# Kernel tuning notes

Hardware: AMD Instinct MI355X
Metric: run time of the kernel (lower is better)

## Reference

```python
import jax, jax.numpy as jnp
import numpy as np
import math

N, C, T, V = 32, 64, 400, 27
S = 2            # num_subset
IC = 16          # inter_channels
EPS = 1e-5


def _spatial_pe(channels, num_node):
    # PositionalEncoding(domain='spatial'): pe[c, t, v] depends only on joint id v
    pos = jnp.arange(num_node, dtype=jnp.float32)                      # [V]
    div = jnp.exp(jnp.arange(0, channels, 2, dtype=jnp.float32)
                  * (-math.log(10000.0) / channels))                   # [C/2]
    ang = div[:, None] * pos[None, :]                                  # [C/2, V]
    pe = jnp.stack([jnp.sin(ang), jnp.cos(ang)], axis=1)               # [C/2, 2, V]
    return pe.reshape(channels, num_node)                              # [C, V]


def _conv1x1(x, w, b):
    # x: [N, Cin, T, V], w: [Cout, Cin]
    return jnp.einsum('nctv,oc->notv', x, w) + b[None, :, None, None]


def _bn(x, g, b, m, v):
    inv = g / jnp.sqrt(v + EPS)
    return x * inv[None, :, None, None] + (b - m * inv)[None, :, None, None]


def _leaky(x):
    return jnp.where(x >= 0, x, 0.1 * x)


def setup_inputs() -> dict:
    key = jax.random.key(0)
    ks = jax.random.split(key, 24)
    d = {}
    d['x'] = jax.random.normal(ks[0], (N, C, T, V), jnp.float32)
    d['w_in'] = jax.random.normal(ks[1], (2 * S * IC, C), jnp.float32) * 0.1
    d['b_in'] = jax.random.normal(ks[2], (2 * S * IC,), jnp.float32) * 0.05
    d['alphas'] = jnp.ones((1, S, 1, 1), jnp.float32)
    d['att0'] = jax.random.uniform(ks[3], (1, S, V, V), jnp.float32) / V
    d['w_outs'] = jax.random.normal(ks[4], (C, S * C), jnp.float32) * 0.08
    d['b_outs'] = jax.random.normal(ks[5], (C,), jnp.float32) * 0.05
    d['bn_outs_g'] = jax.random.uniform(ks[6], (C,), jnp.float32) + 0.5
    d['bn_outs_b'] = jax.random.normal(ks[7], (C,), jnp.float32) * 0.05
    d['bn_outs_m'] = jax.random.normal(ks[8], (C,), jnp.float32) * 0.1
    d['bn_outs_v'] = jax.random.uniform(ks[9], (C,), jnp.float32) + 0.5
    d['w_ff'] = jax.random.normal(ks[10], (C, C), jnp.float32) * 0.1
    d['b_ff'] = jax.random.normal(ks[11], (C,), jnp.float32) * 0.05
    d['bn_ff_g'] = jax.random.uniform(ks[12], (C,), jnp.float32) + 0.5
    d['bn_ff_b'] = jax.random.normal(ks[13], (C,), jnp.float32) * 0.05
    d['bn_ff_m'] = jax.random.normal(ks[14], (C,), jnp.float32) * 0.1
    d['bn_ff_v'] = jax.random.uniform(ks[15], (C,), jnp.float32) + 0.5
    d['w_t'] = jax.random.normal(ks[16], (C, C, 3, 1), jnp.float32) * 0.08
    d['b_t'] = jax.random.normal(ks[17], (C,), jnp.float32) * 0.05
    d['bn_t_g'] = jax.random.uniform(ks[18], (C,), jnp.float32) + 0.5
    d['bn_t_b'] = jax.random.normal(ks[19], (C,), jnp.float32) * 0.05
    d['bn_t_m'] = jax.random.normal(ks[20], (C,), jnp.float32) * 0.1
    d['bn_t_v'] = jax.random.uniform(ks[21], (C,), jnp.float32) + 0.5
    return d


def reference(x, w_in, b_in, alphas, att0,
              w_outs, b_outs, bn_outs_g, bn_outs_b, bn_outs_m, bn_outs_v,
              w_ff, b_ff, bn_ff_g, bn_ff_b, bn_ff_m, bn_ff_v,
              w_t, b_t, bn_t_g, bn_t_b, bn_t_m, bn_t_v):
    n, c, t, v = x.shape
    # spatial positional encoding (broadcast over T)
    pe = _spatial_pe(c, v)                                      # [C, V]
    y = x + pe[None, :, None, :]
    # q/k projection: 1x1 conv -> [N, 2S, IC, T, V], chunk on subset axis
    qk = _conv1x1(y, w_in, b_in).reshape(n, 2 * S, IC, t, v)
    q, k = qk[:, :S], qk[:, S:]
    # tanh attention over joints + learnable global bias (atts buffer is zeros)
    att = jnp.tanh(jnp.einsum('nsctu,nsctv->nsuv', q, k) / (IC * t)) * alphas
    att = att + att0                                            # [N, S, V, V]
    # aggregate V-dim: [N, S, C, T, V] -> [N, S*C, T, V]
    y = jnp.einsum('nctu,nsuv->nsctv', x, att).reshape(n, S * c, t, v)
    y = _bn(_conv1x1(y, w_outs, b_outs), bn_outs_g, bn_outs_b, bn_outs_m, bn_outs_v)
    y = _leaky(x + y)                                           # downs1 = identity
    y2 = _bn(_conv1x1(y, w_ff, b_ff), bn_ff_g, bn_ff_b, bn_ff_m, bn_ff_v)
    y2 = _leaky(x + y2)                                         # downs2 = identity
    # temporal conv (3,1), padding (1,0), stride 1
    z = jax.lax.conv_general_dilated(
        y2, w_t, window_strides=(1, 1), padding=((1, 1), (0, 0)),
        dimension_numbers=('NCHW', 'OIHW', 'NCHW')) + b_t[None, :, None, None]
    z = _bn(z, bn_t_g, bn_t_b, bn_t_m, bn_t_v)
    z = _leaky(y2 + z)                                          # downt2 = identity
    return z
```

## Files before the change

kernel.cpp:

```cpp
#include <hip/hip_runtime.h>
#include <hip/hip_bf16.h>
#include <math.h>


typedef __hip_bfloat16 bf16;
typedef unsigned short u16t;
typedef unsigned int u32t;

using bf16x8 = __attribute__((ext_vector_type(8))) short;
using f32x4  = __attribute__((ext_vector_type(4))) float;

#define NN 32
#define CH 64
#define TT 400
#define VV 27
#define PIX 10800
#define NSUV (32*2*27*27)
#define XTOT (NN*CH*PIX)

#define TB1 4
#define NT1 100
#define TB2 4
#define NT2 100
#define TBS 9
#define NTS 45

__device__ __forceinline__ float lrelu(float x) { return x >= 0.f ? x : 0.1f * x; }
__device__ __forceinline__ float4 ld4(const float* p) { return *reinterpret_cast<const float4*>(p); }
__device__ __forceinline__ uint2 ld2u(const u32t* p) { return *reinterpret_cast<const uint2*>(p); }

__device__ __forceinline__ u16t f2bf(float f) {
    return __bfloat16_as_ushort(__float2bfloat16(f));
}
__device__ __forceinline__ u32t packbf(float lo, float hi) {
    return ((u32t)f2bf(hi) << 16) | (u32t)f2bf(lo);
}
__device__ __forceinline__ float bf2f(u16t u) {
    return __uint_as_float(((u32t)u) << 16);
}
__device__ __forceinline__ u32t cvtpk(float lo, float hi) {
    u32t r;
    asm("v_cvt_pk_bf16_f32 %0, %1, %2" : "=v"(r) : "v"(lo), "v"(hi));
    return r;
}
__device__ __forceinline__ void dot2v(float& c, u32t a, u32t b) {
    asm("v_dot2_f32_bf16 %0, %1, %2, %0" : "+v"(c) : "v"(a), "v"(b));
}
__device__ __forceinline__ void dot2s(float& c, u32t a_sgpr, u32t b) {
    asm("v_dot2_f32_bf16 %0, %1, %2, %0" : "+v"(c) : "s"(a_sgpr), "v"(b));
}

__global__ void k_prep(
    const float* __restrict__ w_outs, const float* __restrict__ b_outs,
    const float* __restrict__ go, const float* __restrict__ bo,
    const float* __restrict__ mo, const float* __restrict__ vo,
    const float* __restrict__ w_ff, const float* __restrict__ b_ff,
    const float* __restrict__ gf, const float* __restrict__ bf,
    const float* __restrict__ mf, const float* __restrict__ vf,
    const float* __restrict__ w_t, const float* __restrict__ b_t,
    const float* __restrict__ gt, const float* __restrict__ btb,
    const float* __restrict__ mt, const float* __restrict__ vt,
    const float* __restrict__ w_in,
    u16t* __restrict__ wfoA, float* __restrict__ bfo,
    u16t* __restrict__ wffA, float* __restrict__ bff,
    u16t* __restrict__ wtA, float* __restrict__ bft,
    u32t* __restrict__ wqkpk)
{
    const int total = 8192 + 4096 + 12288 + 192 + 2048;
    for (int idx = blockIdx.x * 256 + threadIdx.x; idx < total; idx += gridDim.x * 256) {
        if (idx < 8192) {
            int o = idx >> 7, j = idx & 127;
            float inv = go[o] * rsqrtf(vo[o] + 1e-5f);
            wfoA[idx] = f2bf(w_outs[o * 128 + j] * inv);
        } else if (idx < 12288) {
            int r = idx - 8192; int o = r >> 6, c = r & 63;
            float inv = gf[o] * rsqrtf(vf[o] + 1e-5f);
            wffA[r] = f2bf(w_ff[o * 64 + c] * inv);
        } else if (idx < 24576) {
            int r = idx - 12288;
            int o = r / 192, k2 = r % 192;
            int kt = k2 >> 6, c = k2 & 63;
            float inv = gt[o] * rsqrtf(vt[o] + 1e-5f);
            wtA[r] = f2bf(w_t[o * 192 + c * 3 + kt] * inv);
        } else if (idx < 24768) {
            int r = idx - 24576; int o = r & 63, which = r >> 6;
            if (which == 0) {
                float inv = go[o] * rsqrtf(vo[o] + 1e-5f);
                bfo[o] = b_outs[o] * inv + bo[o] - mo[o] * inv;
            } else if (which == 1) {
                float inv = gf[o] * rsqrtf(vf[o] + 1e-5f);
                bff[o] = b_ff[o] * inv + bf[o] - mf[o] * inv;
            } else {
                float inv = gt[o] * rsqrtf(vt[o] + 1e-5f);
                bft[o] = b_t[o] * inv + btb[o] - mt[o] * inv;
            }
        } else {
            int i = idx - 24768;
            int cc2 = i & 31, c = (i >> 5) & 15, sq = i >> 9;
            int s = sq >> 1, qk = sq & 1;
            int row = qk * 32 + s * 16 + c;
            wqkpk[i] = packbf(w_in[row * 64 + 2 * cc2], w_in[row * 64 + 2 * cc2 + 1]);
        }
    }
}

__global__ __launch_bounds__(256) void k_pbias(
    const float* __restrict__ w_in, const float* __restrict__ b_in,
    float* __restrict__ pb)
{
    __shared__ float pe[64 * 27];
    const int tid = threadIdx.x;
    for (int idx = tid; idx < 1728; idx += 256) {
        int c = idx / 27, u = idx % 27;
        float div = expf(-0.28782313662425575f * (float)(c >> 1));
        float ang = div * (float)u;
        pe[idx] = (c & 1) ? cosf(ang) : sinf(ang);
    }
    __syncthreads();
    for (int idx = tid; idx < 1792; idx += 256) {
        int u = idx % 28, r = idx / 28;
        int c = r % 16, sq = r / 16;
        if (u >= 27) { pb[idx] = 0.f; continue; }
        int s = sq >> 1, qk = sq & 1;
        int row = qk * 32 + s * 16 + c;
        float acc = b_in[row];
        for (int cc = 0; cc < 64; ++cc) acc += w_in[row * 64 + cc] * pe[cc * 27 + u];
        pb[idx] = acc;
    }
}

__global__ __launch_bounds__(256, 8) void k_scores(
    const float* __restrict__ x, const u32t* __restrict__ wqkpk,
    const float* __restrict__ pb, float* __restrict__ scores)
{
    const int tid = threadIdx.x;
    const int s = blockIdx.x, n = blockIdx.z;
    const int t0 = blockIdx.y * TBS;

    __shared__ u32t qlds[TBS * 27 * 10];
    __shared__ u32t klds[TBS * 27 * 10];

    const int pcl = tid < 243 ? tid : 242;
    const int tt = pcl / 27, u = pcl - tt * 27;
    const int t = t0 + tt;
    const bool valid = (tid < 243) && (t < TT);

    u32t xp[32];
    const float* xb = x + (size_t)n * 64 * PIX + (size_t)(t < TT ? t : 0) * 27 + u;
    #pragma unroll
    for (int c2 = 0; c2 < 32; ++c2) {
        float v0 = xb[(size_t)(2 * c2) * PIX];
        float v1 = xb[(size_t)(2 * c2 + 1) * PIX];
        xp[c2] = cvtpk(v0, v1);
    }

    const float* pbq = pb + ((s * 2 + 0) * 16) * 28 + u;
    const float* pbk = pb + ((s * 2 + 1) * 16) * 28 + u;
    const u32t* wq = wqkpk + (s * 2 + 0) * 16 * 32;
    const u32t* wk = wqkpk + (s * 2 + 1) * 16 * 32;
    float qr[16], kr[16];
    #pragma unroll
    for (int c = 0; c < 16; ++c) { qr[c] = pbq[c * 28]; kr[c] = pbk[c * 28]; }
    #pragma unroll
    for (int c = 0; c < 16; ++c) {
        const u32t* wr = wq + c * 32;
        #pragma unroll
        for (int c2 = 0; c2 < 32; ++c2) dot2s(qr[c], wr[c2], xp[c2]);
    }
    #pragma unroll
    for (int c = 0; c < 16; ++c) {
        const u32t* wr = wk + c * 32;
        #pragma unroll
        for (int c2 = 0; c2 < 32; ++c2) dot2s(kr[c], wr[c2], xp[c2]);
    }

    if (tid < 243) {
        #pragma unroll
        for (int c2 = 0; c2 < 8; ++c2) {
            qlds[(tt * 27 + u) * 10 + c2] = valid ? cvtpk(qr[2 * c2], qr[2 * c2 + 1]) : 0u;
            klds[(tt * 27 + u) * 10 + c2] = valid ? cvtpk(kr[2 * c2], kr[2 * c2 + 1]) : 0u;
        }
    }
    __syncthreads();

    const int sid = tid < 243 ? tid : 242;
    const int ug = sid / 9, vg = sid % 9;
    const int v0 = vg * 3;
    float sc0 = 0.f, sc1 = 0.f, sc2 = 0.f;
    for (int t2 = 0; t2 < TBS; ++t2) {
        const u32t* qrow = qlds + (t2 * 27 + ug) * 10;
        const u32t* k0 = klds + (t2 * 27 + v0) * 10;
        #pragma unroll
        for (int c4 = 0; c4 < 4; ++c4) {
            uint2 qp = ld2u(qrow + c4 * 2);
            uint2 ka = ld2u(k0 + c4 * 2);
            uint2 kb = ld2u(k0 + 10 + c4 * 2);
            uint2 kc = ld2u(k0 + 20 + c4 * 2);
            dot2v(sc0, qp.x, ka.x); dot2v(sc0, qp.y, ka.y);
            dot2v(sc1, qp.x, kb.x); dot2v(sc1, qp.y, kb.y);
            dot2v(sc2, qp.x, kc.x); dot2v(sc2, qp.y, kc.y);
        }
    }
    if (tid < 243) {
        float* sb = scores + (n * 2 + s) * 729 + ug * 27 + v0;
        atomicAdd(&sb[0], sc0);
        atomicAdd(&sb[1], sc1);
        atomicAdd(&sb[2], sc2);
    }
}

__global__ void k_att(const float* __restrict__ scores,
                      const float* __restrict__ alphas,
                      const float* __restrict__ att0,
                      u32t* __restrict__ attTp)
{
    int i = blockIdx.x * 256 + threadIdx.x;
    if (i >= NN * 2 * 32 * 16) return;
    int e = i & 15;
    int r = i >> 4;
    int v = r & 31;
    int ns = r >> 5;
    int s = ns & 1;
    if (v >= 27) { attTp[i] = 0u; return; }
    const float* sb = scores + ns * 729;
    const float* ab = att0 + s * 729;
    float al = alphas[s];
    int u0 = 2 * e, u1 = 2 * e + 1;
    float a0 = (u0 < 27) ? tanhf(sb[u0 * 27 + v] * (1.f / 6400.f)) * al + ab[u0 * 27 + v] : 0.f;
    float a1 = (u1 < 27) ? tanhf(sb[u1 * 27 + v] * (1.f / 6400.f)) * al + ab[u1 * 27 + v] : 0.f;
    attTp[i] = packbf(a0, a1);
}

__global__ __launch_bounds__(512, 4) void k_stage1(
    const float* __restrict__ x, const u32t* __restrict__ attTp,
    const u16t* __restrict__ wfoA, const float* __restrict__ bfo,
    const u16t* __restrict__ wffA, const float* __restrict__ bff,
    u16t* __restrict__ y2T)
{
    const int tid = threadIdx.x;
    const int n = blockIdx.y, t0 = blockIdx.x * TB1;
    const int w = tid >> 6, li = tid & 15, g = (tid >> 4) & 3;

    __shared__ __align__(16) u16t xs[4 * 64 * 32];
    __shared__ __align__(16) u32t mmL[112 * 68];
    __shared__ __align__(16) u32t y1L[112 * 34];

    for (int j = tid; j < 4096; j += 512) {
        int i = j & 15, c = (j >> 4) & 63, tt = j >> 10;
        const float* xrow = x + (size_t)(n * 64 + c) * PIX + (size_t)(t0 + tt) * 27;
        int u0 = 2 * i;
        float v0 = (u0 < 27) ? xrow[u0] : 0.f;
        float v1 = (u0 + 1 < 27) ? xrow[u0 + 1] : 0.f;
        int ip = i ^ (((c >> 1) & 3) << 2);
        reinterpret_cast<u32t*>(xs)[(tt * 64 + c) * 16 + ip] = packbf(v0, v1);
    }
    __syncthreads();

    {
        const int t = w & 3, s = w >> 2;
        bf16x8 ax[4];
        #pragma unroll
        for (int Mt = 0; Mt < 4; ++Mt) {
            const int c = Mt * 16 + li;
            const int blk = g ^ ((li >> 1) & 3);
            ax[Mt] = *reinterpret_cast<const bf16x8*>(&xs[(t * 64 + c) * 32 + blk * 8]);
        }
        const u16t* attp16 = reinterpret_cast<const u16t*>(attTp);
        #pragma unroll
        for (int Nt = 0; Nt < 2; ++Nt) {
            bf16x8 b = *reinterpret_cast<const bf16x8*>(
                &attp16[(((n * 2 + s) * 32) + Nt * 16 + li) * 32 + g * 8]);
            const int v = Nt * 16 + li;
            #pragma unroll
            for (int Mt = 0; Mt < 4; ++Mt) {
                f32x4 d = {0.f, 0.f, 0.f, 0.f};
                d = __builtin_amdgcn_mfma_f32_16x16x32_bf16(ax[Mt], b, d, 0, 0, 0);
                if (v < 28) {
                    const int p = t * 28 + v;
                    const int j2 = s * 32 + Mt * 8 + g * 2;
                    mmL[p * 68 + j2]     = packbf(d[0], d[1]);
                    mmL[p * 68 + j2 + 1] = packbf(d[2], d[3]);
                }
            }
        }
    }
    __syncthreads();

    const int ot = w & 3, hh = w >> 2;
    const int o0 = ot * 16 + g * 4;

    {
        bf16x8 aw[4];
        #pragma unroll
        for (int Ks = 0; Ks < 4; ++Ks)
            aw[Ks] = *reinterpret_cast<const bf16x8*>(&wfoA[(ot * 16 + li) * 128 + Ks * 32 + g * 8]);
        float4 bf4 = ld4(&bfo[o0]);
        #pragma unroll
        for (int q = 0; q < 4; ++q) {
            const int Nt = hh * 4 + q;
            if (Nt >= 7) continue;
            f32x4 d = {0.f, 0.f, 0.f, 0.f};
            #pragma unroll
            for (int Ks = 0; Ks < 4; ++Ks) {
                bf16x8 b = *reinterpret_cast<const bf16x8*>(&mmL[(Nt * 16 + li) * 68 + Ks * 16 + g * 4]);
                d = __builtin_amdgcn_mfma_f32_16x16x32_bf16(aw[Ks], b, d, 0, 0, 0);
            }
            const int p = Nt * 16 + li;
            const int tt = p / 28, v = p - tt * 28;
            const int sw0 = ((o0 >> 1) & 3) << 3;
            const int sw1 = (((o0 + 2) >> 1) & 3) << 3;
            float ya = lrelu(bf2f(xs[(tt * 64 + o0 + 0) * 32 + (v ^ sw0)]) + d[0] + bf4.x);
            float yb = lrelu(bf2f(xs[(tt * 64 + o0 + 1) * 32 + (v ^ sw0)]) + d[1] + bf4.y);
            float yc = lrelu(bf2f(xs[(tt * 64 + o0 + 2) * 32 + (v ^ sw1)]) + d[2] + bf4.z);
            float yd = lrelu(bf2f(xs[(tt * 64 + o0 + 3) * 32 + (v ^ sw1)]) + d[3] + bf4.w);
            y1L[p * 34 + ot * 8 + g * 2]     = packbf(ya, yb);
            y1L[p * 34 + ot * 8 + g * 2 + 1] = packbf(yc, yd);
        }
    }
    __syncthreads();

    {
        bf16x8 af[2];
        #pragma unroll
        for (int Ks = 0; Ks < 2; ++Ks)
            af[Ks] = *reinterpret_cast<const bf16x8*>(&wffA[(ot * 16 + li) * 64 + Ks * 32 + g * 8]);
        float4 bff4 = ld4(&bff[o0]);
        #pragma unroll
        for (int q = 0; q < 4; ++q) {
            const int Nt = hh * 4 + q;
            if (Nt >= 7) continue;
            f32x4 d = {0.f, 0.f, 0.f, 0.f};
            #pragma unroll
            for (int Ks = 0; Ks < 2; ++Ks) {
                union { uint2 u2[2]; bf16x8 v8; } bu;
                bu.u2[0] = *reinterpret_cast<const uint2*>(&y1L[(Nt * 16 + li) * 34 + Ks * 16 + g * 4]);
                bu.u2[1] = *reinterpret_cast<const uint2*>(&y1L[(Nt * 16 + li) * 34 + Ks * 16 + g * 4 + 2]);
                d = __builtin_amdgcn_mfma_f32_16x16x32_bf16(af[Ks], bu.v8, d, 0, 0, 0);
            }
            const int p = Nt * 16 + li;
            const int tt = p / 28, v = p - tt * 28;
            if (v < 27) {
                const int sw0 = ((o0 >> 1) & 3) << 3;
                const int sw1 = (((o0 + 2) >> 1) & 3) << 3;
                float r0 = lrelu(bf2f(xs[(tt * 64 + o0 + 0) * 32 + (v ^ sw0)]) + d[0] + bff4.x);
                float r1 = lrelu(bf2f(xs[(tt * 64 + o0 + 1) * 32 + (v ^ sw0)]) + d[1] + bff4.y);
                float r2 = lrelu(bf2f(xs[(tt * 64 + o0 + 2) * 32 + (v ^ sw1)]) + d[2] + bff4.z);
                float r3 = lrelu(bf2f(xs[(tt * 64 + o0 + 3) * 32 + (v ^ sw1)]) + d[3] + bff4.w);
                uint2 st;
                st.x = packbf(r0, r1);
                st.y = packbf(r2, r3);
                size_t P = (size_t)n * PIX + (size_t)(t0 + tt) * 27 + v;
                *reinterpret_cast<uint2*>(y2T + P * 64 + o0) = st;
            }
        }
    }
}

__global__ __launch_bounds__(256, 4) void k_stage2(
    const u16t* __restrict__ y2T, const u16t* __restrict__ wtA,
    const float* __restrict__ bft, float* __restrict__ out)
{
    const int tid = threadIdx.x;
    const int n = blockIdx.y, t0 = blockIdx.x * TB2;
    const int w = tid >> 6, li = tid & 15, g = (tid >> 4) & 3;

    __shared__ __align__(16) u16t ys[6 * 28 * 72];

    for (int idx = tid; idx < 6 * 27 * 8; idx += 256) {
        int q = idx & 7, r = idx >> 3;
        int v = r % 27, tp = r / 27;
        int t = t0 - 1 + tp;
        uint4 val = {0u, 0u, 0u, 0u};
        if (t >= 0 && t < TT)
            val = *reinterpret_cast<const uint4*>(
                &y2T[((size_t)n * PIX + (size_t)t * 27 + v) * 64 + q * 8]);
        *reinterpret_cast<uint4*>(&ys[(tp * 28 + v) * 72 + q * 8]) = val;
    }
    for (int idx = tid; idx < 6 * 8; idx += 256) {
        int q = idx & 7, tp = idx >> 3;
        uint4 z = {0u, 0u, 0u, 0u};
        *reinterpret_cast<uint4*>(&ys[(tp * 28 + 27) * 72 + q * 8]) = z;
    }
    __syncthreads();

    const int o0 = w * 16 + g * 4;
    bf16x8 aw[6];
    #pragma unroll
    for (int Ks = 0; Ks < 6; ++Ks)
        aw[Ks] = *reinterpret_cast<const bf16x8*>(&wtA[(w * 16 + li) * 192 + Ks * 32 + g * 8]);
    float4 bt4 = ld4(&bft[o0]);

    #pragma unroll
    for (int Nt = 0; Nt < 7; ++Nt) {
        const int p = Nt * 16 + li;
        const int tt = p / 28, v = p - tt * 28;
        f32x4 d = {0.f, 0.f, 0.f, 0.f};
        #pragma unroll
        for (int Ks = 0; Ks < 6; ++Ks) {
            const int kt = Ks >> 1, c0 = (Ks & 1) * 32 + g * 8;
            bf16x8 b = *reinterpret_cast<const bf16x8*>(&ys[((tt + kt) * 28 + v) * 72 + c0]);
            d = __builtin_amdgcn_mfma_f32_16x16x32_bf16(aw[Ks], b, d, 0, 0, 0);
        }
        if (v < 27) {
            float* ob = out + (size_t)(n * 64) * PIX + (size_t)(t0 + tt) * 27 + v;
            float r0 = bf2f(ys[((tt + 1) * 28 + v) * 72 + o0 + 0]);
            float r1 = bf2f(ys[((tt + 1) * 28 + v) * 72 + o0 + 1]);
            float r2 = bf2f(ys[((tt + 1) * 28 + v) * 72 + o0 + 2]);
            float r3 = bf2f(ys[((tt + 1) * 28 + v) * 72 + o0 + 3]);
            ob[(size_t)(o0 + 0) * PIX] = lrelu(r0 + d[0] + bt4.x);
            ob[(size_t)(o0 + 1) * PIX] = lrelu(r1 + d[1] + bt4.y);
            ob[(size_t)(o0 + 2) * PIX] = lrelu(r2 + d[2] + bt4.z);
            ob[(size_t)(o0 + 3) * PIX] = lrelu(r3 + d[3] + bt4.w);
        }
    }
}

extern "C" void kernel_launch(void* const* d_in, const int* in_sizes, int n_in,
                              void* d_out, int out_size, void* d_ws, size_t ws_size,
                              hipStream_t stream)
{
    const float* x      = (const float*)d_in[0];
    const float* w_in   = (const float*)d_in[1];
    const float* b_in   = (const float*)d_in[2];
    const float* alphas = (const float*)d_in[3];
    const float* att0   = (const float*)d_in[4];
    const float* w_outs = (const float*)d_in[5];
    const float* b_outs = (const float*)d_in[6];
    const float* bog    = (const float*)d_in[7];
    const float* bob    = (const float*)d_in[8];
    const float* bom    = (const float*)d_in[9];
    const float* bov    = (const float*)d_in[10];
    const float* w_ff   = (const float*)d_in[11];
    const float* b_ff   = (const float*)d_in[12];
    const float* bfg    = (const float*)d_in[13];
    const float* bfb    = (const float*)d_in[14];
    const float* bfm    = (const float*)d_in[15];
    const float* bfv    = (const float*)d_in[16];
    const float* w_t    = (const float*)d_in[17];
    const float* b_t    = (const float*)d_in[18];
    const float* btg    = (const float*)d_in[19];
    const float* btb    = (const float*)d_in[20];
    const float* btm    = (const float*)d_in[21];
    const float* btv    = (const float*)d_in[22];

    float* pbw    = (float*)d_ws;
    float* scores = pbw + 1792;
    u32t*  attTp  = (u32t*)(scores + NSUV);
    u16t*  wfoA   = (u16t*)(attTp + 32768);
    u16t*  wffA   = (u16t*)((u32t*)wfoA + 4096);
    u16t*  wtA    = (u16t*)((u32t*)wffA + 2048);
    float* bfo    = (float*)((u32t*)wtA + 6144);
    float* bff    = bfo + 64;
    float* bft    = bff + 64;
    u32t*  wqkpk  = (u32t*)(bft + 64);
    u16t*  y2T    = (u16t*)(wqkpk + 2048);

    hipMemsetAsync(scores, 0, NSUV * sizeof(float), stream);

    k_prep<<<32, 256, 0, stream>>>(w_outs, b_outs, bog, bob, bom, bov,
                                   w_ff, b_ff, bfg, bfb, bfm, bfv,
                                   w_t, b_t, btg, btb, btm, btv, w_in,
                                   wfoA, bfo, wffA, bff, wtA, bft, wqkpk);
    k_pbias<<<1, 256, 0, stream>>>(w_in, b_in, pbw);
    k_scores<<<dim3(2, NTS, NN), 256, 0, stream>>>(x, wqkpk, pbw, scores);
    k_att<<<(NN * 2 * 32 * 16 + 255) / 256, 256, 0, stream>>>(scores, alphas, att0, attTp);
    k_stage1<<<dim3(NT1, NN), 512, 0, stream>>>(x, attTp, wfoA, bfo, wffA, bff, y2T);
    k_stage2<<<dim3(NT2, NN), 256, 0, stream>>>(y2T, wtA, bft, (float*)d_out);
}
```

Before: 399.7 us.

## Rewrite attention-score kernel to use MFMA for QK projection and scores

The scores kernel now stages an 8-timestep x tile in LDS as bf16 in a transposed layout. It computes the q/k projections with 16x16x32 bf16 MFMA instructions instead of per-thread scalar dot2 loops, and then computes the 27x27 q·k^T partial scores with MFMA over padded 32x32 tiles. This is meant to cut the VALU-bound dot-product work and the per-thread register pressure. In exchange it adds padding waste, extra LDS traffic and more blocks (50 time tiles instead of 45), and it lowers the launch-bounds occupancy hint.

```diff
diff --git a/kernel.cpp b/kernel.cpp
--- a/kernel.cpp
+++ b/kernel.cpp
@@ -22,12 +22,11 @@
 #define NT1 100
 #define TB2 4
 #define NT2 100
-#define TBS 9
-#define NTS 45
+#define TB_S 8
+#define NT_S 50
 
 __device__ __forceinline__ float lrelu(float x) { return x >= 0.f ? x : 0.1f * x; }
 __device__ __forceinline__ float4 ld4(const float* p) { return *reinterpret_cast<const float4*>(p); }
-__device__ __forceinline__ uint2 ld2u(const u32t* p) { return *reinterpret_cast<const uint2*>(p); }
 
 __device__ __forceinline__ u16t f2bf(float f) {
     return __bfloat16_as_ushort(__float2bfloat16(f));
@@ -42,12 +41,6 @@
     u32t r;
     asm("v_cvt_pk_bf16_f32 %0, %1, %2" : "=v"(r) : "v"(lo), "v"(hi));
     return r;
-}
-__device__ __forceinline__ void dot2v(float& c, u32t a, u32t b) {
-    asm("v_dot2_f32_bf16 %0, %1, %2, %0" : "+v"(c) : "v"(a), "v"(b));
-}
-__device__ __forceinline__ void dot2s(float& c, u32t a_sgpr, u32t b) {
-    asm("v_dot2_f32_bf16 %0, %1, %2, %0" : "+v"(c) : "s"(a_sgpr), "v"(b));
 }
 
 __global__ void k_prep(
@@ -129,83 +122,102 @@
     }
 }
 
-__global__ __launch_bounds__(256, 8) void k_scores(
+__global__ __launch_bounds__(256, 3) void k_scores(
     const float* __restrict__ x, const u32t* __restrict__ wqkpk,
     const float* __restrict__ pb, float* __restrict__ scores)
 {
     const int tid = threadIdx.x;
     const int s = blockIdx.x, n = blockIdx.z;
-    const int t0 = blockIdx.y * TBS;
-
-    __shared__ u32t qlds[TBS * 27 * 10];
-    __shared__ u32t klds[TBS * 27 * 10];
-
-    const int pcl = tid < 243 ? tid : 242;
-    const int tt = pcl / 27, u = pcl - tt * 27;
-    const int t = t0 + tt;
-    const bool valid = (tid < 243) && (t < TT);
-
-    u32t xp[32];
-    const float* xb = x + (size_t)n * 64 * PIX + (size_t)(t < TT ? t : 0) * 27 + u;
-    #pragma unroll
-    for (int c2 = 0; c2 < 32; ++c2) {
-        float v0 = xb[(size_t)(2 * c2) * PIX];
-        float v1 = xb[(size_t)(2 * c2 + 1) * PIX];
-        xp[c2] = cvtpk(v0, v1);
-    }
-
-    const float* pbq = pb + ((s * 2 + 0) * 16) * 28 + u;
-    const float* pbk = pb + ((s * 2 + 1) * 16) * 28 + u;
-    const u32t* wq = wqkpk + (s * 2 + 0) * 16 * 32;
-    const u32t* wk = wqkpk + (s * 2 + 1) * 16 * 32;
-    float qr[16], kr[16];
-    #pragma unroll
-    for (int c = 0; c < 16; ++c) { qr[c] = pbq[c * 28]; kr[c] = pbk[c * 28]; }
-    #pragma unroll
-    for (int c = 0; c < 16; ++c) {
-        const u32t* wr = wq + c * 32;
-        #pragma unroll
-        for (int c2 = 0; c2 < 32; ++c2) dot2s(qr[c], wr[c2], xp[c2]);
-    }
-    #pragma unroll
-    for (int c = 0; c < 16; ++c) {
-        const u32t* wr = wk + c * 32;
-        #pragma unroll
-        for (int c2 = 0; c2 < 32; ++c2) dot2s(kr[c], wr[c2], xp[c2]);
-    }
-
-    if (tid < 243) {
-        #pragma unroll
-        for (int c2 = 0; c2 < 8; ++c2) {
-            qlds[(tt * 27 + u) * 10 + c2] = valid ? cvtpk(qr[2 * c2], qr[2 * c2 + 1]) : 0u;
-            klds[(tt * 27 + u) * 10 + c2] = valid ? cvtpk(kr[2 * c2], kr[2 * c2 + 1]) : 0u;
-        }
-    }
-    __syncthreads();
-
-    const int sid = tid < 243 ? tid : 242;
-    const int ug = sid / 9, vg = sid % 9;
-    const int v0 = vg * 3;
-    float sc0 = 0.f, sc1 = 0.f, sc2 = 0.f;
-    for (int t2 = 0; t2 < TBS; ++t2) {
-        const u32t* qrow = qlds + (t2 * 27 + ug) * 10;
-        const u32t* k0 = klds + (t2 * 27 + v0) * 10;
-        #pragma unroll
-        for (int c4 = 0; c4 < 4; ++c4) {
-            uint2 qp = ld2u(qrow + c4 * 2);
-            uint2 ka = ld2u(k0 + c4 * 2);
-            uint2 kb = ld2u(k0 + 10 + c4 * 2);
-            uint2 kc = ld2u(k0 + 20 + c4 * 2);
-            dot2v(sc0, qp.x, ka.x); dot2v(sc0, qp.y, ka.y);
-            dot2v(sc1, qp.x, kb.x); dot2v(sc1, qp.y, kb.y);
-            dot2v(sc2, qp.x, kc.x); dot2v(sc2, qp.y, kc.y);
-        }
-    }
-    if (tid < 243) {
-        float* sb = scores + (n * 2 + s) * 729 + ug * 27 + v0;
-        atomicAdd(&sb[0], sc0);
-        atomicAdd(&sb[1], sc1);
-        atomicAdd(&sb[2], sc2);
+    const int t0 = blockIdx.y * TB_S;
+    const int w = tid >> 6, li = tid & 15, g = (tid >> 4) & 3;
+
+    __shared__ __align__(16) u16t xT[224 * 72];
+    __shared__ __align__(16) u16t qL[8 * 32 * 16];
+    __shared__ __align__(16) u16t kL[8 * 32 * 16];
+
+    u32t* xT32 = reinterpret_cast<u32t*>(xT);
+    u32t* qL32 = reinterpret_cast<u32t*>(qL);
+    u32t* kL32 = reinterpret_cast<u32t*>(kL);
+
+    for (int idx = tid; idx < 224 * 32; idx += 256) {
+        int p = idx % 224, c2 = idx / 224;
+        u32t val = 0u;
+        if (p < 216) {
+            const float* xp = x + ((size_t)(n * 64 + 2 * c2)) * PIX + (size_t)t0 * 27 + p;
+            val = cvtpk(xp[0], xp[PIX]);
+        }
+        xT32[p * 36 + c2] = val;
+    }
+    for (int idx = tid; idx < 640; idx += 256) {
+        int buf = idx / 320, r = idx - buf * 320;
+        int t = r / 40, rr = r - t * 40;
+        int uu = 27 + rr / 8, wq = rr - (rr / 8) * 8;
+        (buf ? kL32 : qL32)[(t * 32 + uu) * 8 + wq] = 0u;
+    }
+    __syncthreads();
+
+    {
+        bf16x8 aq[2], ak[2];
+        #pragma unroll
+        for (int Ks = 0; Ks < 2; ++Ks) {
+            aq[Ks] = *reinterpret_cast<const bf16x8*>(
+                &wqkpk[((s * 2 + 0) * 16 + li) * 32 + Ks * 16 + g * 4]);
+            ak[Ks] = *reinterpret_cast<const bf16x8*>(
+                &wqkpk[((s * 2 + 1) * 16 + li) * 32 + Ks * 16 + g * 4]);
+        }
+        const float* pbq = pb + ((s * 2 + 0) * 16) * 28;
+        const float* pbk = pb + ((s * 2 + 1) * 16) * 28;
+        for (int Nt = w; Nt < 14; Nt += 4) {
+            f32x4 dq = {0.f, 0.f, 0.f, 0.f}, dk = {0.f, 0.f, 0.f, 0.f};
+            #pragma unroll
+            for (int Ks = 0; Ks < 2; ++Ks) {
+                bf16x8 b = *reinterpret_cast<const bf16x8*>(
+                    &xT[(Nt * 16 + li) * 72 + Ks * 32 + g * 8]);
+                dq = __builtin_amdgcn_mfma_f32_16x16x32_bf16(aq[Ks], b, dq, 0, 0, 0);
+                dk = __builtin_amdgcn_mfma_f32_16x16x32_bf16(ak[Ks], b, dk, 0, 0, 0);
+            }
+            const int p = Nt * 16 + li;
+            if (p < 216) {
+                const int t = p / 27, u = p - t * 27;
+                const int c0 = g * 4;
+                float q0 = dq[0] + pbq[(c0 + 0) * 28 + u];
+                float q1 = dq[1] + pbq[(c0 + 1) * 28 + u];
+                float q2 = dq[2] + pbq[(c0 + 2) * 28 + u];
+                float q3 = dq[3] + pbq[(c0 + 3) * 28 + u];
+                float k0 = dk[0] + pbk[(c0 + 0) * 28 + u];
+                float k1 = dk[1] + pbk[(c0 + 1) * 28 + u];
+                float k2 = dk[2] + pbk[(c0 + 2) * 28 + u];
+                float k3 = dk[3] + pbk[(c0 + 3) * 28 + u];
+                qL32[(t * 32 + u) * 8 + g * 2]     = packbf(q0, q1);
+                qL32[(t * 32 + u) * 8 + g * 2 + 1] = packbf(q2, q3);
+                kL32[(t * 32 + u) * 8 + g * 2]     = packbf(k0, k1);
+                kL32[(t * 32 + u) * 8 + g * 2 + 1] = packbf(k2, k3);
+            }
+        }
+    }
+    __syncthreads();
+
+    {
+        const int Mt = w >> 1, Nt = w & 1;
+        f32x4 d = {0.f, 0.f, 0.f, 0.f};
+        #pragma unroll
+        for (int Ks = 0; Ks < 4; ++Ks) {
+            const int t = Ks * 2 + (g >> 1), cp = (g & 1) * 8;
+            bf16x8 a = *reinterpret_cast<const bf16x8*>(
+                &qL[(t * 32 + Mt * 16 + li) * 16 + cp]);
+            bf16x8 b = *reinterpret_cast<const bf16x8*>(
+                &kL[(t * 32 + Nt * 16 + li) * 16 + cp]);
+            d = __builtin_amdgcn_mfma_f32_16x16x32_bf16(a, b, d, 0, 0, 0);
+        }
+        const int v = Nt * 16 + li;
+        if (v < 27) {
+            float* sb = scores + (n * 2 + s) * 729;
+            #pragma unroll
+            for (int r = 0; r < 4; ++r) {
+                const int u = Mt * 16 + g * 4 + r;
+                if (u < 27) atomicAdd(&sb[u * 27 + v], d[r]);
+            }
+        }
     }
 }
 
@@ -462,7 +474,7 @@
                                    w_t, b_t, btg, btb, btm, btv, w_in,
                                    wfoA, bfo, wffA, bff, wtA, bft, wqkpk);
     k_pbias<<<1, 256, 0, stream>>>(w_in, b_in, pbw);
-    k_scores<<<dim3(2, NTS, NN), 256, 0, stream>>>(x, wqkpk, pbw, scores);
+    k_scores<<<dim3(2, NT_S, NN), 256, 0, stream>>>(x, wqkpk, pbw, scores);
     k_att<<<(NN * 2 * 32 * 16 + 255) / 256, 256, 0, stream>>>(scores, alphas, att0, attTp);
     k_stage1<<<dim3(NT1, NN), 512, 0, stream>>>(x, attTp, wfoA, bfo, wffA, bff, y2T);
     k_stage2<<<dim3(NT2, NN), 256, 0, stream>>>(y2T, wtA, bft, (float*)d_out);
```

Result: no change. 406.0 us (+1.6%).
